# Kernel optimization log

Hardware: AMD Instinct MI355X
Metric: run time of the kernel (lower is better)

## Reference

```python
import jax, jax.numpy as jnp
import numpy as np

MAX_FEATURES = 5000
EMBED_DIM = 100
H1, H2, NUM_CLASSES = 64, 32, 4
BATCH, SEQ = 1024, 256


def _keras_lstm_scan(x_seq, mask_seq, W, U, b):
    """x_seq: [T,B,E], mask_seq: [T,B] bool. Keras gate order i,f,c,o.
    Masked steps carry (h, c) through unchanged (Keras mask_zero semantics).
    Returns (all hidden states [T,B,H], final hidden [B,H])."""
    B = x_seq.shape[1]
    H = U.shape[0]
    h0 = jnp.zeros((B, H), x_seq.dtype)
    c0 = jnp.zeros((B, H), x_seq.dtype)

    def step(carry, inp):
        h, c = carry
        x, m = inp
        z = x @ W + h @ U + b  # [B, 4H]
        i, f, g, o = jnp.split(z, 4, axis=-1)
        i = jax.nn.sigmoid(i)
        f = jax.nn.sigmoid(f)
        g = jnp.tanh(g)
        o = jax.nn.sigmoid(o)
        c_new = f * c + i * g
        h_new = o * jnp.tanh(c_new)
        m = m[:, None]
        h2 = jnp.where(m, h_new, h)
        c2 = jnp.where(m, c_new, c)
        return (h2, c2), h2

    (hT, _), hs = jax.lax.scan(step, (h0, c0), (x_seq, mask_seq))
    return hs, hT


def setup_inputs() -> dict:
    key = jax.random.key(0)
    ks = jax.random.split(key, 8)
    s = 0.05
    tokens = jax.random.randint(ks[0], (BATCH, SEQ), 0, MAX_FEATURES, dtype=jnp.int32)
    emb = jax.random.normal(ks[1], (MAX_FEATURES, EMBED_DIM), jnp.float32) * s
    W1 = jax.random.normal(ks[2], (EMBED_DIM, 4 * H1), jnp.float32) * s
    U1 = jax.random.normal(ks[3], (H1, 4 * H1), jnp.float32) * s
    b1 = jnp.zeros((4 * H1,), jnp.float32)
    W2 = jax.random.normal(ks[4], (H1, 4 * H2), jnp.float32) * s
    U2 = jax.random.normal(ks[5], (H2, 4 * H2), jnp.float32) * s
    b2 = jnp.zeros((4 * H2,), jnp.float32)
    Wd = jax.random.normal(ks[6], (H2, NUM_CLASSES), jnp.float32) * s
    bd = jnp.zeros((NUM_CLASSES,), jnp.float32)
    return {"tokens": tokens, "emb": emb, "W1": W1, "U1": U1, "b1": b1,
            "W2": W2, "U2": U2, "b2": b2, "Wd": Wd, "bd": bd}


def reference(tokens, emb, W1, U1, b1, W2, U2, b2, Wd, bd):
    mask = (tokens != 0)                       # [B,T] mask_zero=True
    x = emb[tokens]                            # [B,T,E]
    x_t = jnp.transpose(x, (1, 0, 2))          # [T,B,E]
    m_t = jnp.transpose(mask, (1, 0))          # [T,B]
    hs1, _ = _keras_lstm_scan(x_t, m_t, W1, U1, b1)   # [T,B,64]
    _, h2 = _keras_lstm_scan(hs1, m_t, W2, U2, b2)    # [B,32] last valid state
    return jax.nn.sigmoid(h2 @ Wd + bd)        # [B,4]
```

## Files before the change

kernel.cpp:

```cpp
#include <hip/hip_runtime.h>

typedef _Float16 hp2 __attribute__((ext_vector_type(2)));

#define NB    1024
#define TT    256
#define EE    100
#define VOCAB 5000
#define GG1   256
#define GG2   128

__device__ __forceinline__ float fast_sigmoid(float x) {
  return __builtin_amdgcn_rcpf(1.0f + __expf(-x));
}
__device__ __forceinline__ float fast_tanh(float x) {
  return 1.0f - 2.0f * __builtin_amdgcn_rcpf(1.0f + __expf(2.0f * x));
}

__global__ __launch_bounds__(256) void emb_gemm(
    const float* __restrict__ emb, const float* __restrict__ W1,
    const float* __restrict__ b1, float* __restrict__ emb_zi)
{
  __shared__ float sE[8][EE];
  const int j  = threadIdx.x;
  const int v0 = blockIdx.x * 8;
  for (int idx = j; idx < 8 * EE; idx += 256) {
    int r = idx / EE, k = idx % EE;
    sE[r][k] = emb[(size_t)(v0 + r) * EE + k];
  }
  __syncthreads();
  float acc[8];
  const float bb = b1[j];
  #pragma unroll
  for (int r = 0; r < 8; ++r) acc[r] = bb;
  for (int k = 0; k < EE; ++k) {
    float w = W1[k * GG1 + j];
    #pragma unroll
    for (int r = 0; r < 8; ++r) acc[r] = fmaf(sE[r][k], w, acc[r]);
  }
  const int slot = (j & 63) * 4 + (j >> 6);
  #pragma unroll
  for (int r = 0; r < 8; ++r) emb_zi[(size_t)(v0 + r) * GG1 + slot] = acc[r];
}

__global__ __launch_bounds__(64) __attribute__((amdgpu_waves_per_eu(1, 1)))
void lstm_row(
    const int* __restrict__ tokens, const float* __restrict__ emb_zi,
    const float* __restrict__ U1,
    const float* __restrict__ W2, const float* __restrict__ U2, const float* __restrict__ b2,
    const float* __restrict__ Wd, const float* __restrict__ bd,
    float* __restrict__ out)
{
  __shared__ __align__(16) _Float16 sHB[2][96];
  __shared__ int sTok[TT];

  const int u   = threadIdx.x;
  const int row = blockIdx.x;
  const int u2  = u & 31;
  const int s   = u >> 5;

  hp2 wA[128];
  #pragma unroll
  for (int p = 0; p < 32; ++p) {
    #pragma unroll
    for (int g = 0; g < 4; ++g) {
      hp2 w;
      w[0] = (_Float16)U1[(2 * p + 0) * GG1 + g * 64 + u];
      w[1] = (_Float16)U1[(2 * p + 1) * GG1 + g * 64 + u];
      wA[4 * p + g] = w;
    }
  }
  hp2 wB[96];
  #pragma unroll
  for (int p = 0; p < 24; ++p) {
    int k0 = 48 * s + 2 * p;
    const float* r0 = (k0     < 64) ? &W2[(size_t)k0 * GG2]       : &U2[(size_t)(k0 - 64) * GG2];
    const float* r1 = (k0 + 1 < 64) ? &W2[(size_t)(k0 + 1) * GG2] : &U2[(size_t)(k0 + 1 - 64) * GG2];
    #pragma unroll
    for (int g = 0; g < 4; ++g) {
      hp2 w;
      w[0] = (_Float16)r0[g * 32 + u2];
      w[1] = (_Float16)r1[g * 32 + u2];
      wB[4 * p + g] = w;
    }
  }
  const float bi2 = b2[u2], bf2 = b2[32 + u2], bg2 = b2[64 + u2], bo2 = b2[96 + u2];

  ((int4*)sTok)[u] = ((const int4*)(tokens + (size_t)row * TT))[u];
  sHB[0][u] = (_Float16)0.0f;
  sHB[1][u] = (_Float16)0.0f;
  if (u < 32) { sHB[0][64 + u] = (_Float16)0.0f; sHB[1][64 + u] = (_Float16)0.0f; }
  __syncthreads();

  float c1 = 0.f, h1r = 0.f, c2 = 0.f, h2r = 0.f;

  int tok_b = sTok[0];
  {
    float4 zx0 = *(const float4*)&emb_zi[(size_t)tok_b * GG1 + 4 * u];
    if (tok_b != 0) {
      float iv = fast_sigmoid(zx0.x), fv = fast_sigmoid(zx0.y);
      float gv = fast_tanh(zx0.z),    ov = fast_sigmoid(zx0.w);
      (void)fv;
      c1 = iv * gv; h1r = ov * fast_tanh(c1);
    }
    sHB[0][u] = (_Float16)h1r;
  }
  int   tok_a = sTok[1];
  float4 zxa = *(const float4*)&emb_zi[(size_t)tok_a * GG1 + 4 * u];
  __syncthreads();

  for (int t = 0; t < TT; ++t) {
    const _Float16* rb = sHB[t & 1];
    _Float16*       wb = (_Float16*)sHB[(t & 1) ^ 1];

    int tok_n = 0;
    float4 zxn = zxa;
    if (t + 2 < TT) {
      tok_n = sTok[t + 2];
      zxn = *(const float4*)&emb_zi[(size_t)tok_n * GG1 + 4 * u];
    }

    float a0 = zxa.x, a1 = zxa.y, a2 = zxa.z, a3 = zxa.w;
    #pragma unroll
    for (int q = 0; q < 8; ++q) {
      int4 hq = ((const int4*)rb)[q];
      #pragma unroll
      for (int pp = 0; pp < 4; ++pp) {
        hp2 hv = ((const hp2*)&hq)[pp];
        const int p = 4 * q + pp;
        a0 = __builtin_amdgcn_fdot2(hv, wA[4 * p + 0], a0, false);
        a1 = __builtin_amdgcn_fdot2(hv, wA[4 * p + 1], a1, false);
        a2 = __builtin_amdgcn_fdot2(hv, wA[4 * p + 2], a2, false);
        a3 = __builtin_amdgcn_fdot2(hv, wA[4 * p + 3], a3, false);
      }
    }

    float b0 = 0.f, b1v = 0.f, b2v = 0.f, b3 = 0.f;
    const int4* hbp = (const int4*)(rb + 48 * s);
    #pragma unroll
    for (int q = 0; q < 6; ++q) {
      int4 hq = hbp[q];
      #pragma unroll
      for (int pp = 0; pp < 4; ++pp) {
        hp2 hv = ((const hp2*)&hq)[pp];
        const int p = 4 * q + pp;
        b0  = __builtin_amdgcn_fdot2(hv, wB[4 * p + 0], b0,  false);
        b1v = __builtin_amdgcn_fdot2(hv, wB[4 * p + 1], b1v, false);
        b2v = __builtin_amdgcn_fdot2(hv, wB[4 * p + 2], b2v, false);
        b3  = __builtin_amdgcn_fdot2(hv, wB[4 * p + 3], b3,  false);
      }
    }

    b0  += __shfl_xor(b0, 32);
    b1v += __shfl_xor(b1v, 32);
    b2v += __shfl_xor(b2v, 32);
    b3  += __shfl_xor(b3, 32);
    {
      const bool mb = (tok_b != 0);
      float i2 = fast_sigmoid(b0 + bi2);
      float f2 = fast_sigmoid(b1v + bf2);
      float g2 = fast_tanh(b2v + bg2);
      float o2 = fast_sigmoid(b3 + bo2);
      if (mb) { c2 = f2 * c2 + i2 * g2; h2r = o2 * fast_tanh(c2); }
    }
    if (s == 0) wb[64 + u2] = (_Float16)h2r;

    {
      const bool ma = (tok_a != 0);
      float iv = fast_sigmoid(a0);
      float fv = fast_sigmoid(a1);
      float gv = fast_tanh(a2);
      float ov = fast_sigmoid(a3);
      if (ma) { c1 = fv * c1 + iv * gv; h1r = ov * fast_tanh(c1); }
    }
    wb[u] = (_Float16)h1r;
    __syncthreads();

    tok_b = tok_a; tok_a = tok_n; zxa = zxn;
  }

  if (u < 4) {
    float a = bd[u];
    #pragma unroll
    for (int k = 0; k < 32; ++k)
      a = fmaf((float)sHB[0][64 + k], Wd[k * 4 + u], a);
    out[(size_t)row * 4 + u] = fast_sigmoid(a);
  }
}

extern "C" void kernel_launch(void* const* d_in, const int* in_sizes, int n_in,
                              void* d_out, int out_size, void* d_ws, size_t ws_size,
                              hipStream_t stream) {
  const int*   tokens = (const int*)d_in[0];
  const float* emb    = (const float*)d_in[1];
  const float* W1     = (const float*)d_in[2];
  const float* U1     = (const float*)d_in[3];
  const float* b1     = (const float*)d_in[4];
  const float* W2     = (const float*)d_in[5];
  const float* U2     = (const float*)d_in[6];
  const float* b2     = (const float*)d_in[7];
  const float* Wd     = (const float*)d_in[8];
  const float* bd     = (const float*)d_in[9];
  float* out    = (float*)d_out;
  float* emb_zi = (float*)d_ws;

  emb_gemm<<<dim3(VOCAB / 8), dim3(256), 0, stream>>>(emb, W1, b1, emb_zi);
  lstm_row<<<dim3(NB), dim3(64), 0, stream>>>(
      tokens, emb_zi, U1, W2, U2, b2, Wd, bd, out);
}
```

Measured before the change: 251.8 us.

## Split LSTM layers across two wavefronts with per-step barrier handoff

Each row block now uses two waves: wave 0 runs the layer-1 recurrence and wave 1 runs the layer-2 recurrence. They exchange hidden states through double-buffered shared memory and synchronise with a custom s_barrier each step. The aim is to run the two layers' dot products and activations concurrently instead of serially in one wave, which shortens the per-step critical path. In exchange it needs a barrier between waves every step and launches twice as many threads per block.

```diff
diff --git a/kernel.cpp b/kernel.cpp
--- a/kernel.cpp
+++ b/kernel.cpp
@@ -14,6 +14,12 @@
 }
 __device__ __forceinline__ float fast_tanh(float x) {
   return 1.0f - 2.0f * __builtin_amdgcn_rcpf(1.0f + __expf(2.0f * x));
+}
+
+__device__ __forceinline__ void step_sync() {
+  asm volatile("s_waitcnt lgkmcnt(0)" ::: "memory");
+  __builtin_amdgcn_s_barrier();
+  __builtin_amdgcn_sched_barrier(0);
 }
 
 __global__ __launch_bounds__(256) void emb_gemm(
@@ -42,8 +48,8 @@
   for (int r = 0; r < 8; ++r) emb_zi[(size_t)(v0 + r) * GG1 + slot] = acc[r];
 }
 
-__global__ __launch_bounds__(64) __attribute__((amdgpu_waves_per_eu(1, 1)))
-void lstm_row(
+__global__ __launch_bounds__(128) __attribute__((amdgpu_waves_per_eu(2, 2)))
+void lstm_dual(
     const int* __restrict__ tokens, const float* __restrict__ emb_zi,
     const float* __restrict__ U1,
     const float* __restrict__ W2, const float* __restrict__ U2, const float* __restrict__ b2,
@@ -53,137 +59,143 @@
   __shared__ __align__(16) _Float16 sHB[2][96];
   __shared__ int sTok[TT];
 
-  const int u   = threadIdx.x;
+  const int tid = threadIdx.x;
+  const int u   = tid & 63;
+  const int wv  = tid >> 6;
   const int row = blockIdx.x;
-  const int u2  = u & 31;
-  const int s   = u >> 5;
-
-  hp2 wA[128];
-  #pragma unroll
-  for (int p = 0; p < 32; ++p) {
-    #pragma unroll
-    for (int g = 0; g < 4; ++g) {
-      hp2 w;
-      w[0] = (_Float16)U1[(2 * p + 0) * GG1 + g * 64 + u];
-      w[1] = (_Float16)U1[(2 * p + 1) * GG1 + g * 64 + u];
-      wA[4 * p + g] = w;
-    }
-  }
-  hp2 wB[96];
-  #pragma unroll
-  for (int p = 0; p < 24; ++p) {
-    int k0 = 48 * s + 2 * p;
-    const float* r0 = (k0     < 64) ? &W2[(size_t)k0 * GG2]       : &U2[(size_t)(k0 - 64) * GG2];
-    const float* r1 = (k0 + 1 < 64) ? &W2[(size_t)(k0 + 1) * GG2] : &U2[(size_t)(k0 + 1 - 64) * GG2];
-    #pragma unroll
-    for (int g = 0; g < 4; ++g) {
-      hp2 w;
-      w[0] = (_Float16)r0[g * 32 + u2];
-      w[1] = (_Float16)r1[g * 32 + u2];
-      wB[4 * p + g] = w;
-    }
-  }
-  const float bi2 = b2[u2], bf2 = b2[32 + u2], bg2 = b2[64 + u2], bo2 = b2[96 + u2];
-
-  ((int4*)sTok)[u] = ((const int4*)(tokens + (size_t)row * TT))[u];
-  sHB[0][u] = (_Float16)0.0f;
-  sHB[1][u] = (_Float16)0.0f;
-  if (u < 32) { sHB[0][64 + u] = (_Float16)0.0f; sHB[1][64 + u] = (_Float16)0.0f; }
+
+  ((int2*)sTok)[tid] = ((const int2*)(tokens + (size_t)row * TT))[tid];
+  if (tid < 96) { sHB[0][tid] = (_Float16)0.0f; sHB[1][tid] = (_Float16)0.0f; }
+
+  if (wv == 0) {
+    hp2 wA[128];
+    #pragma unroll
+    for (int p = 0; p < 32; ++p) {
+      #pragma unroll
+      for (int g = 0; g < 4; ++g) {
+        hp2 w;
+        w[0] = (_Float16)U1[(2 * p + 0) * GG1 + g * 64 + u];
+        w[1] = (_Float16)U1[(2 * p + 1) * GG1 + g * 64 + u];
+        wA[4 * p + g] = w;
+      }
+    }
+    __syncthreads();
+
+    float c1 = 0.f, h1r = 0.f;
+    {
+      int tok0 = sTok[0];
+      float4 zx0 = *(const float4*)&emb_zi[(size_t)tok0 * GG1 + 4 * u];
+      if (tok0 != 0) {
+        float iv = fast_sigmoid(zx0.x);
+        float gv = fast_tanh(zx0.z);
+        float ov = fast_sigmoid(zx0.w);
+        c1 = iv * gv; h1r = ov * fast_tanh(c1);
+      }
+      sHB[0][u] = (_Float16)h1r;
+    }
+    int   tok_a = sTok[1];
+    float4 zxa = *(const float4*)&emb_zi[(size_t)tok_a * GG1 + 4 * u];
+    step_sync();
+
+    for (int t = 0; t < TT; ++t) {
+      if (t + 1 < TT) {
+        float a0 = zxa.x, a1 = zxa.y, a2 = zxa.z, a3 = zxa.w;
+        int tok_n = 0;
+        if (t + 2 < TT) {
+          tok_n = sTok[t + 2];
+          zxa = *(const float4*)&emb_zi[(size_t)tok_n * GG1 + 4 * u];
+        }
+        const int4* rb = (const int4*)&sHB[t & 1][0];
+        #pragma unroll
+        for (int q = 0; q < 8; ++q) {
+          int4 hq = rb[q];
+          #pragma unroll
+          for (int pp = 0; pp < 4; ++pp) {
+            const int p = 4 * q + pp;
+            hp2 hv = ((const hp2*)&hq)[pp];
+            a0 = __builtin_amdgcn_fdot2(hv, wA[4 * p + 0], a0, false);
+            a1 = __builtin_amdgcn_fdot2(hv, wA[4 * p + 1], a1, false);
+            a2 = __builtin_amdgcn_fdot2(hv, wA[4 * p + 2], a2, false);
+            a3 = __builtin_amdgcn_fdot2(hv, wA[4 * p + 3], a3, false);
+          }
+        }
+        {
+          const bool ma = (tok_a != 0);
+          float iv = fast_sigmoid(a0);
+          float fv = fast_sigmoid(a1);
+          float gv = fast_tanh(a2);
+          float ov = fast_sigmoid(a3);
+          if (ma) { c1 = fv * c1 + iv * gv; h1r = ov * fast_tanh(c1); }
+        }
+        sHB[(t & 1) ^ 1][u] = (_Float16)h1r;
+        tok_a = tok_n;
+      }
+      step_sync();
+    }
+  } else {
+    const int u2 = u & 31;
+    const int s  = u >> 5;
+    hp2 wB[96];
+    #pragma unroll
+    for (int p = 0; p < 24; ++p) {
+      int k0 = 48 * s + 2 * p;
+      const float* r0 = (k0     < 64) ? &W2[(size_t)k0 * GG2]       : &U2[(size_t)(k0 - 64) * GG2];
+      const float* r1 = (k0 + 1 < 64) ? &W2[(size_t)(k0 + 1) * GG2] : &U2[(size_t)(k0 + 1 - 64) * GG2];
+      #pragma unroll
+      for (int g = 0; g < 4; ++g) {
+        hp2 w;
+        w[0] = (_Float16)r0[g * 32 + u2];
+        w[1] = (_Float16)r1[g * 32 + u2];
+        wB[4 * p + g] = w;
+      }
+    }
+    const float bi2 = b2[u2], bf2 = b2[32 + u2], bg2 = b2[64 + u2], bo2 = b2[96 + u2];
+    __syncthreads();
+
+    float c2 = 0.f, h2r = 0.f;
+    step_sync();
+
+    for (int t = 0; t < TT; ++t) {
+      const int tok_b = sTok[t];
+      float b0 = 0.f, b1v = 0.f, b2v = 0.f, b3 = 0.f;
+      const int4* hbp = (const int4*)(&sHB[t & 1][48 * s]);
+      #pragma unroll
+      for (int q = 0; q < 6; ++q) {
+        int4 hq = hbp[q];
+        #pragma unroll
+        for (int pp = 0; pp < 4; ++pp) {
+          const int p = 4 * q + pp;
+          hp2 hv = ((const hp2*)&hq)[pp];
+          b0  = __builtin_amdgcn_fdot2(hv, wB[4 * p + 0], b0,  false);
+          b1v = __builtin_amdgcn_fdot2(hv, wB[4 * p + 1], b1v, false);
+          b2v = __builtin_amdgcn_fdot2(hv, wB[4 * p + 2], b2v, false);
+          b3  = __builtin_amdgcn_fdot2(hv, wB[4 * p + 3], b3,  false);
+        }
+      }
+      b0  += __shfl_xor(b0, 32);
+      b1v += __shfl_xor(b1v, 32);
+      b2v += __shfl_xor(b2v, 32);
+      b3  += __shfl_xor(b3, 32);
+      {
+        const bool mb = (tok_b != 0);
+        float i2 = fast_sigmoid(b0 + bi2);
+        float f2 = fast_sigmoid(b1v + bf2);
+        float g2 = fast_tanh(b2v + bg2);
+        float o2 = fast_sigmoid(b3 + bo2);
+        if (mb) { c2 = f2 * c2 + i2 * g2; h2r = o2 * fast_tanh(c2); }
+      }
+      if (s == 0) sHB[(t & 1) ^ 1][64 + u2] = (_Float16)h2r;
+      step_sync();
+    }
+  }
   __syncthreads();
 
-  float c1 = 0.f, h1r = 0.f, c2 = 0.f, h2r = 0.f;
-
-  int tok_b = sTok[0];
-  {
-    float4 zx0 = *(const float4*)&emb_zi[(size_t)tok_b * GG1 + 4 * u];
-    if (tok_b != 0) {
-      float iv = fast_sigmoid(zx0.x), fv = fast_sigmoid(zx0.y);
-      float gv = fast_tanh(zx0.z),    ov = fast_sigmoid(zx0.w);
-      (void)fv;
-      c1 = iv * gv; h1r = ov * fast_tanh(c1);
-    }
-    sHB[0][u] = (_Float16)h1r;
-  }
-  int   tok_a = sTok[1];
-  float4 zxa = *(const float4*)&emb_zi[(size_t)tok_a * GG1 + 4 * u];
-  __syncthreads();
-
-  for (int t = 0; t < TT; ++t) {
-    const _Float16* rb = sHB[t & 1];
-    _Float16*       wb = (_Float16*)sHB[(t & 1) ^ 1];
-
-    int tok_n = 0;
-    float4 zxn = zxa;
-    if (t + 2 < TT) {
-      tok_n = sTok[t + 2];
-      zxn = *(const float4*)&emb_zi[(size_t)tok_n * GG1 + 4 * u];
-    }
-
-    float a0 = zxa.x, a1 = zxa.y, a2 = zxa.z, a3 = zxa.w;
-    #pragma unroll
-    for (int q = 0; q < 8; ++q) {
-      int4 hq = ((const int4*)rb)[q];
-      #pragma unroll
-      for (int pp = 0; pp < 4; ++pp) {
-        hp2 hv = ((const hp2*)&hq)[pp];
-        const int p = 4 * q + pp;
-        a0 = __builtin_amdgcn_fdot2(hv, wA[4 * p + 0], a0, false);
-        a1 = __builtin_amdgcn_fdot2(hv, wA[4 * p + 1], a1, false);
-        a2 = __builtin_amdgcn_fdot2(hv, wA[4 * p + 2], a2, false);
-        a3 = __builtin_amdgcn_fdot2(hv, wA[4 * p + 3], a3, false);
-      }
-    }
-
-    float b0 = 0.f, b1v = 0.f, b2v = 0.f, b3 = 0.f;
-    const int4* hbp = (const int4*)(rb + 48 * s);
-    #pragma unroll
-    for (int q = 0; q < 6; ++q) {
-      int4 hq = hbp[q];
-      #pragma unroll
-      for (int pp = 0; pp < 4; ++pp) {
-        hp2 hv = ((const hp2*)&hq)[pp];
-        const int p = 4 * q + pp;
-        b0  = __builtin_amdgcn_fdot2(hv, wB[4 * p + 0], b0,  false);
-        b1v = __builtin_amdgcn_fdot2(hv, wB[4 * p + 1], b1v, false);
-        b2v = __builtin_amdgcn_fdot2(hv, wB[4 * p + 2], b2v, false);
-        b3  = __builtin_amdgcn_fdot2(hv, wB[4 * p + 3], b3,  false);
-      }
-    }
-
-    b0  += __shfl_xor(b0, 32);
-    b1v += __shfl_xor(b1v, 32);
-    b2v += __shfl_xor(b2v, 32);
-    b3  += __shfl_xor(b3, 32);
-    {
-      const bool mb = (tok_b != 0);
-      float i2 = fast_sigmoid(b0 + bi2);
-      float f2 = fast_sigmoid(b1v + bf2);
-      float g2 = fast_tanh(b2v + bg2);
-      float o2 = fast_sigmoid(b3 + bo2);
-      if (mb) { c2 = f2 * c2 + i2 * g2; h2r = o2 * fast_tanh(c2); }
-    }
-    if (s == 0) wb[64 + u2] = (_Float16)h2r;
-
-    {
-      const bool ma = (tok_a != 0);
-      float iv = fast_sigmoid(a0);
-      float fv = fast_sigmoid(a1);
-      float gv = fast_tanh(a2);
-      float ov = fast_sigmoid(a3);
-      if (ma) { c1 = fv * c1 + iv * gv; h1r = ov * fast_tanh(c1); }
-    }
-    wb[u] = (_Float16)h1r;
-    __syncthreads();
-
-    tok_b = tok_a; tok_a = tok_n; zxa = zxn;
-  }
-
-  if (u < 4) {
-    float a = bd[u];
+  if (tid < 4) {
+    float a = bd[tid];
     #pragma unroll
     for (int k = 0; k < 32; ++k)
-      a = fmaf((float)sHB[0][64 + k], Wd[k * 4 + u], a);
-    out[(size_t)row * 4 + u] = fast_sigmoid(a);
+      a = fmaf((float)sHB[0][64 + k], Wd[k * 4 + tid], a);
+    out[(size_t)row * 4 + tid] = fast_sigmoid(a);
   }
 }
 
@@ -204,6 +216,6 @@
   float* emb_zi = (float*)d_ws;
 
   emb_gemm<<<dim3(VOCAB / 8), dim3(256), 0, stream>>>(emb, W1, b1, emb_zi);
-  lstm_row<<<dim3(NB), dim3(64), 0, stream>>>(
+  lstm_dual<<<dim3(NB), dim3(128), 0, stream>>>(
       tokens, emb_zi, U1, W2, U2, b2, Wd, bd, out);
 }
```

New measurement: 223.1 us. 11.4% less time.
